# Optimization experiments

Measured on AMD Instinct MI355X. Metric: run time of the kernel, lower is better.

Reference implementation:

```python
import jax, jax.numpy as jnp
import numpy as np

EPS = 1e-6  # torch.nn.CosineSimilarity eps


def setup_inputs() -> dict:
    key = jax.random.key(0)
    k1, k2, k3, k4 = jax.random.split(key, 4)
    B, S, I, H, P = 16, 512, 512, 512, 16
    hidden = jax.random.normal(k1, (B, S, I), dtype=jnp.float32)
    # per-prototype linear weights (no bias); torch Linear stores (out, in)
    W1 = jax.random.normal(k2, (P, H, I), dtype=jnp.float32) / np.sqrt(I)
    W2 = jax.random.normal(k3, (P, H, H), dtype=jnp.float32) / np.sqrt(H)
    protos = jax.random.normal(k4, (P, H), dtype=jnp.float32)  # torch.randn(1,H) per proto
    return {"hidden": hidden, "W1": W1, "W2": W2, "protos": protos}


def reference(hidden, W1, W2, protos):
    # Batched version of the per-prototype loop:
    # layer1: ReLU(hidden @ W1[p].T) -> [B,S,P,H]
    h1 = jax.nn.relu(jnp.einsum("bsi,phi->bsph", hidden, W1))
    # layer2: ReLU(h1 @ W2[p].T) -> [B,S,P,H]
    h2 = jax.nn.relu(jnp.einsum("bsph,pgh->bspg", h1, W2))
    # cosine similarity along feature dim vs. each prototype vector
    dot = jnp.einsum("bsph,ph->bsp", h2, protos)
    xn = jnp.maximum(jnp.linalg.norm(h2, axis=-1), EPS)          # [B,S,P]
    pn = jnp.maximum(jnp.linalg.norm(protos, axis=-1), EPS)      # [P]
    cos_scores = dot / (xn * pn)                                  # [B,S,P]
    return cos_scores
```

## Files before the change

### kernel.cpp

```cpp
#include <hip/hip_runtime.h>
#include <hip/hip_bf16.h>

#define R_TOT 8192
#define DIM   512
#define NP    16
#define EPSV  1e-6f

typedef __bf16 bf16x8 __attribute__((ext_vector_type(8)));
typedef float  f32x16 __attribute__((ext_vector_type(16)));

__device__ __forceinline__ unsigned int f2bf(float f) {
  unsigned int u = __float_as_uint(f);
  return (u + 0x7FFFu + ((u >> 16) & 1u)) >> 16;
}
__device__ __forceinline__ unsigned int pack2(float a, float b) {
  return f2bf(a) | (f2bf(b) << 16);
}
__device__ __forceinline__ f32x16 zero16() {
  f32x16 z;
  #pragma unroll
  for (int i = 0; i < 16; ++i) z[i] = 0.f;
  return z;
}

__global__ void cvt_x_kernel(const float* __restrict__ X, unsigned short* __restrict__ Xb) {
  int t   = blockIdx.x * 256 + threadIdx.x;
  int row = t >> 6;
  int c   = t & 63;
  const float4* src = (const float4*)(X + (size_t)row * DIM + c * 8);
  float4 f0 = src[0], f1 = src[1];
  uint4 o;
  o.x = pack2(f0.x, f0.y);
  o.y = pack2(f0.z, f0.w);
  o.z = pack2(f1.x, f1.y);
  o.w = pack2(f1.z, f1.w);
  *(uint4*)(Xb + (size_t)row * DIM + 8 * (c ^ (row & 7))) = o;
}

__global__ void pack_w_kernel(const float* __restrict__ W, unsigned short* __restrict__ Wp) {
  int t  = blockIdx.x * 256 + threadIdx.x;
  int l  = t & 63;
  int kk = (t >> 6) & 31;
  int mt = (t >> 11) & 15;
  int p  = t >> 15;
  int row = mt * 32 + (l & 31);
  int k0  = 16 * kk + 8 * (l >> 5);
  const float4* s = (const float4*)(W + ((size_t)p * DIM + row) * DIM + k0);
  float4 f0 = s[0], f1 = s[1];
  uint4 o;
  o.x = pack2(f0.x, f0.y);
  o.y = pack2(f0.z, f0.w);
  o.z = pack2(f1.x, f1.y);
  o.w = pack2(f1.z, f1.w);
  *(uint4*)(Wp + (size_t)t * 8) = o;
}

__global__ void proto_norm_kernel(const float* __restrict__ protos, float* __restrict__ pn) {
  int p = blockIdx.x;
  int l = threadIdx.x;
  float ss = 0.f;
  #pragma unroll
  for (int k = 0; k < DIM / 64; ++k) {
    float v = protos[p * DIM + k * 64 + l];
    ss += v * v;
  }
  #pragma unroll
  for (int m = 32; m >= 1; m >>= 1) ss += __shfl_xor(ss, m, 64);
  if (l == 0) pn[p] = fmaxf(sqrtf(ss), EPSV);
}

__device__ __forceinline__ void gemm_stage32(const unsigned short* tile,
                                             const unsigned short* __restrict__ Wpk,
                                             f32x16 acc[2][2],
                                             int l, int l31, int h) {
  for (int kk = 0; kk < 32; ++kk) {
    bf16x8 a[2], b[2];
    #pragma unroll
    for (int mi = 0; mi < 2; ++mi)
      a[mi] = *(const bf16x8*)(Wpk + (size_t)mi * 16384 + kk * 512 + l * 8);
    #pragma unroll
    for (int nt = 0; nt < 2; ++nt) {
      int token = nt * 32 + l31;
      int boff  = (32 * kk + 16 * h) ^ ((token & 7) << 4);
      b[nt] = *(const bf16x8*)((const char*)tile + token * 1024 + boff);
    }
    #pragma unroll
    for (int mi = 0; mi < 2; ++mi)
      #pragma unroll
      for (int nt = 0; nt < 2; ++nt)
        acc[mi][nt] = __builtin_amdgcn_mfma_f32_32x32x16_bf16(a[mi], b[nt], acc[mi][nt], 0, 0, 0);
  }
}

__global__ __launch_bounds__(512, 4) void fused_kernel(
    const unsigned short* __restrict__ Xb,
    const unsigned short* __restrict__ W1p,
    const unsigned short* __restrict__ W2p,
    const float* __restrict__ protos,
    const float* __restrict__ pn,
    float* __restrict__ out) {
  __shared__ unsigned short tile[64 * DIM];
  __shared__ float red[8][64][2];

  const int raw = blockIdx.x;
  const int bid = (raw & 7) * 256 + (raw >> 3);
  const int p   = bid >> 7;
  const int r0  = (bid & 127) << 6;
  const int tid = threadIdx.x;
  const int w   = tid >> 6;
  const int l   = tid & 63;
  const int l31 = l & 31;
  const int h   = l >> 5;

  {
    const uint4* g = (const uint4*)(Xb + (size_t)r0 * DIM);
    uint4* s = (uint4*)tile;
    #pragma unroll
    for (int it = 0; it < 8; ++it) s[tid + it * 512] = g[tid + it * 512];
  }
  __syncthreads();

  f32x16 acc[2][2];
  #pragma unroll
  for (int mi = 0; mi < 2; ++mi)
    #pragma unroll
    for (int nt = 0; nt < 2; ++nt) acc[mi][nt] = zero16();

  gemm_stage32(tile, W1p + ((size_t)p * 16 + 2 * w) * 16384, acc, l, l31, h);

  __syncthreads();

  #pragma unroll
  for (int mi = 0; mi < 2; ++mi)
    #pragma unroll
    for (int nt = 0; nt < 2; ++nt) {
      int token = nt * 32 + l31;
      #pragma unroll
      for (int g = 0; g < 4; ++g) {
        uint2 pk;
        pk.x = pack2(fmaxf(acc[mi][nt][4 * g + 0], 0.f), fmaxf(acc[mi][nt][4 * g + 1], 0.f));
        pk.y = pack2(fmaxf(acc[mi][nt][4 * g + 2], 0.f), fmaxf(acc[mi][nt][4 * g + 3], 0.f));
        int featb = 128 * w + 64 * mi + 16 * g + 8 * h;
        *(uint2*)((char*)tile + token * 1024 + (featb ^ ((token & 7) << 4))) = pk;
      }
    }
  __syncthreads();

  #pragma unroll
  for (int mi = 0; mi < 2; ++mi)
    #pragma unroll
    for (int nt = 0; nt < 2; ++nt) acc[mi][nt] = zero16();

  gemm_stage32(tile, W2p + ((size_t)p * 16 + 2 * w) * 16384, acc, l, l31, h);

  #pragma unroll
  for (int nt = 0; nt < 2; ++nt) {
    float d = 0.f, ssq = 0.f;
    #pragma unroll
    for (int mi = 0; mi < 2; ++mi)
      #pragma unroll
      for (int g = 0; g < 4; ++g) {
        float4 pv = *(const float4*)(protos + p * DIM + 64 * w + 32 * mi + 8 * g + 4 * h);
        #pragma unroll
        for (int j = 0; j < 4; ++j) {
          float hv = fmaxf(acc[mi][nt][4 * g + j], 0.f);
          d   += hv * ((const float*)&pv)[j];
          ssq += hv * hv;
        }
      }
    d   += __shfl_xor(d, 32, 64);
    ssq += __shfl_xor(ssq, 32, 64);
    if (l < 32) {
      red[w][nt * 32 + l31][0] = d;
      red[w][nt * 32 + l31][1] = ssq;
    }
  }
  __syncthreads();

  if (tid < 64) {
    float d = 0.f, ssq = 0.f;
    #pragma unroll
    for (int ww = 0; ww < 8; ++ww) {
      d   += red[ww][tid][0];
      ssq += red[ww][tid][1];
    }
    float xn = fmaxf(sqrtf(ssq), EPSV);
    out[(size_t)(r0 + tid) * NP + p] = d / (xn * pn[p]);
  }
}

extern "C" void kernel_launch(void* const* d_in, const int* in_sizes, int n_in,
                              void* d_out, int out_size, void* d_ws, size_t ws_size,
                              hipStream_t stream) {
  const float* X      = (const float*)d_in[0];
  const float* W1     = (const float*)d_in[1];
  const float* W2     = (const float*)d_in[2];
  const float* protos = (const float*)d_in[3];
  float* out = (float*)d_out;

  unsigned short* Xb  = (unsigned short*)d_ws;
  unsigned short* W1p = Xb  + (size_t)R_TOT * DIM;
  unsigned short* W2p = W1p + (size_t)NP * DIM * DIM;
  float* pn = (float*)(W2p + (size_t)NP * DIM * DIM);

  cvt_x_kernel<<<2048, 256, 0, stream>>>(X, Xb);
  pack_w_kernel<<<2048, 256, 0, stream>>>(W1, W1p);
  pack_w_kernel<<<2048, 256, 0, stream>>>(W2, W2p);
  proto_norm_kernel<<<NP, 64, 0, stream>>>(protos, pn);
  fused_kernel<<<2048, 512, 0, stream>>>(Xb, W1p, W2p, protos, pn, out);
}
```

Before: 165.8 us.

## Double token tile to 128 rows and software-pipeline GEMM operand loads

Each block now processes 128 token rows instead of 64, so every weight fragment loaded from global memory feeds four MFMA tiles rather than two. This halves the weight traffic per output and the grid shrinks to 1024 blocks. The k-loop also prefetches A and B fragments two steps ahead through a 3-deep register ring. The reduction scratch now reuses the tile buffer after a barrier. In exchange the shared tile grows to 128 KB, occupancy bound drops to 2 blocks, and register pressure rises with 8 accumulators plus prefetch buffers.

```diff
diff --git a/kernel.cpp b/kernel.cpp
--- a/kernel.cpp
+++ b/kernel.cpp
@@ -71,41 +71,58 @@
 
 __device__ __forceinline__ void gemm_stage32(const unsigned short* tile,
                                              const unsigned short* __restrict__ Wpk,
-                                             f32x16 acc[2][2],
+                                             f32x16 acc[2][4],
                                              int l, int l31, int h) {
+  const char* tbase = (const char*)tile;
+  bf16x8 a[3][2], b[3][4];
+  #pragma unroll
+  for (int pp = 0; pp < 2; ++pp) {
+    #pragma unroll
+    for (int mi = 0; mi < 2; ++mi)
+      a[pp][mi] = *(const bf16x8*)(Wpk + (size_t)mi * 16384 + pp * 512 + l * 8);
+    #pragma unroll
+    for (int nt = 0; nt < 4; ++nt) {
+      int token = nt * 32 + l31;
+      int boff  = (32 * pp + 16 * h) ^ ((token & 7) << 4);
+      b[pp][nt] = *(const bf16x8*)(tbase + token * 1024 + boff);
+    }
+  }
+  #pragma unroll
   for (int kk = 0; kk < 32; ++kk) {
-    bf16x8 a[2], b[2];
+    const int cur = kk % 3;
+    const int nxt = (kk + 2) % 3;
+    if (kk + 2 < 32) {
+      #pragma unroll
+      for (int mi = 0; mi < 2; ++mi)
+        a[nxt][mi] = *(const bf16x8*)(Wpk + (size_t)mi * 16384 + (kk + 2) * 512 + l * 8);
+      #pragma unroll
+      for (int nt = 0; nt < 4; ++nt) {
+        int token = nt * 32 + l31;
+        int boff  = (32 * (kk + 2) + 16 * h) ^ ((token & 7) << 4);
+        b[nxt][nt] = *(const bf16x8*)(tbase + token * 1024 + boff);
+      }
+    }
     #pragma unroll
     for (int mi = 0; mi < 2; ++mi)
-      a[mi] = *(const bf16x8*)(Wpk + (size_t)mi * 16384 + kk * 512 + l * 8);
-    #pragma unroll
-    for (int nt = 0; nt < 2; ++nt) {
-      int token = nt * 32 + l31;
-      int boff  = (32 * kk + 16 * h) ^ ((token & 7) << 4);
-      b[nt] = *(const bf16x8*)((const char*)tile + token * 1024 + boff);
-    }
-    #pragma unroll
-    for (int mi = 0; mi < 2; ++mi)
-      #pragma unroll
-      for (int nt = 0; nt < 2; ++nt)
-        acc[mi][nt] = __builtin_amdgcn_mfma_f32_32x32x16_bf16(a[mi], b[nt], acc[mi][nt], 0, 0, 0);
-  }
-}
-
-__global__ __launch_bounds__(512, 4) void fused_kernel(
+      #pragma unroll
+      for (int nt = 0; nt < 4; ++nt)
+        acc[mi][nt] = __builtin_amdgcn_mfma_f32_32x32x16_bf16(a[cur][mi], b[cur][nt], acc[mi][nt], 0, 0, 0);
+  }
+}
+
+__global__ __launch_bounds__(512, 2) void fused_kernel(
     const unsigned short* __restrict__ Xb,
     const unsigned short* __restrict__ W1p,
     const unsigned short* __restrict__ W2p,
     const float* __restrict__ protos,
     const float* __restrict__ pn,
     float* __restrict__ out) {
-  __shared__ unsigned short tile[64 * DIM];
-  __shared__ float red[8][64][2];
+  __shared__ unsigned short tile[128 * DIM];
 
   const int raw = blockIdx.x;
-  const int bid = (raw & 7) * 256 + (raw >> 3);
-  const int p   = bid >> 7;
-  const int r0  = (bid & 127) << 6;
+  const int bid = (raw & 7) * 128 + (raw >> 3);
+  const int p   = bid >> 6;
+  const int r0  = (bid & 63) << 7;
   const int tid = threadIdx.x;
   const int w   = tid >> 6;
   const int l   = tid & 63;
@@ -114,17 +131,17 @@
 
   {
     const uint4* g = (const uint4*)(Xb + (size_t)r0 * DIM);
-    uint4* s = (uint4*)tile;
-    #pragma unroll
-    for (int it = 0; it < 8; ++it) s[tid + it * 512] = g[tid + it * 512];
-  }
-  __syncthreads();
-
-  f32x16 acc[2][2];
+    uint4* sm = (uint4*)tile;
+    #pragma unroll
+    for (int it = 0; it < 16; ++it) sm[tid + it * 512] = g[tid + it * 512];
+  }
+  __syncthreads();
+
+  f32x16 acc[2][4];
   #pragma unroll
   for (int mi = 0; mi < 2; ++mi)
     #pragma unroll
-    for (int nt = 0; nt < 2; ++nt) acc[mi][nt] = zero16();
+    for (int nt = 0; nt < 4; ++nt) acc[mi][nt] = zero16();
 
   gemm_stage32(tile, W1p + ((size_t)p * 16 + 2 * w) * 16384, acc, l, l31, h);
 
@@ -133,14 +150,14 @@
   #pragma unroll
   for (int mi = 0; mi < 2; ++mi)
     #pragma unroll
-    for (int nt = 0; nt < 2; ++nt) {
+    for (int nt = 0; nt < 4; ++nt) {
       int token = nt * 32 + l31;
       #pragma unroll
-      for (int g = 0; g < 4; ++g) {
+      for (int gg = 0; gg < 4; ++gg) {
         uint2 pk;
-        pk.x = pack2(fmaxf(acc[mi][nt][4 * g + 0], 0.f), fmaxf(acc[mi][nt][4 * g + 1], 0.f));
-        pk.y = pack2(fmaxf(acc[mi][nt][4 * g + 2], 0.f), fmaxf(acc[mi][nt][4 * g + 3], 0.f));
-        int featb = 128 * w + 64 * mi + 16 * g + 8 * h;
+        pk.x = pack2(fmaxf(acc[mi][nt][4 * gg + 0], 0.f), fmaxf(acc[mi][nt][4 * gg + 1], 0.f));
+        pk.y = pack2(fmaxf(acc[mi][nt][4 * gg + 2], 0.f), fmaxf(acc[mi][nt][4 * gg + 3], 0.f));
+        int featb = 128 * w + 64 * mi + 16 * gg + 8 * h;
         *(uint2*)((char*)tile + token * 1024 + (featb ^ ((token & 7) << 4))) = pk;
       }
     }
@@ -149,40 +166,48 @@
   #pragma unroll
   for (int mi = 0; mi < 2; ++mi)
     #pragma unroll
-    for (int nt = 0; nt < 2; ++nt) acc[mi][nt] = zero16();
+    for (int nt = 0; nt < 4; ++nt) acc[mi][nt] = zero16();
 
   gemm_stage32(tile, W2p + ((size_t)p * 16 + 2 * w) * 16384, acc, l, l31, h);
 
-  #pragma unroll
-  for (int nt = 0; nt < 2; ++nt) {
+  float dv[4], sv[4];
+  #pragma unroll
+  for (int nt = 0; nt < 4; ++nt) {
     float d = 0.f, ssq = 0.f;
     #pragma unroll
     for (int mi = 0; mi < 2; ++mi)
       #pragma unroll
-      for (int g = 0; g < 4; ++g) {
-        float4 pv = *(const float4*)(protos + p * DIM + 64 * w + 32 * mi + 8 * g + 4 * h);
+      for (int gg = 0; gg < 4; ++gg) {
+        float4 pv = *(const float4*)(protos + p * DIM + 64 * w + 32 * mi + 8 * gg + 4 * h);
         #pragma unroll
         for (int j = 0; j < 4; ++j) {
-          float hv = fmaxf(acc[mi][nt][4 * g + j], 0.f);
+          float hv = fmaxf(acc[mi][nt][4 * gg + j], 0.f);
           d   += hv * ((const float*)&pv)[j];
           ssq += hv * hv;
         }
       }
     d   += __shfl_xor(d, 32, 64);
     ssq += __shfl_xor(ssq, 32, 64);
+    dv[nt] = d;
+    sv[nt] = ssq;
+  }
+
+  __syncthreads();
+  float* red = (float*)tile;
+  #pragma unroll
+  for (int nt = 0; nt < 4; ++nt)
     if (l < 32) {
-      red[w][nt * 32 + l31][0] = d;
-      red[w][nt * 32 + l31][1] = ssq;
-    }
-  }
-  __syncthreads();
-
-  if (tid < 64) {
+      red[(w * 128 + nt * 32 + l31) * 2 + 0] = dv[nt];
+      red[(w * 128 + nt * 32 + l31) * 2 + 1] = sv[nt];
+    }
+  __syncthreads();
+
+  if (tid < 128) {
     float d = 0.f, ssq = 0.f;
     #pragma unroll
     for (int ww = 0; ww < 8; ++ww) {
-      d   += red[ww][tid][0];
-      ssq += red[ww][tid][1];
+      d   += red[(ww * 128 + tid) * 2 + 0];
+      ssq += red[(ww * 128 + tid) * 2 + 1];
     }
     float xn = fmaxf(sqrtf(ssq), EPSV);
     out[(size_t)(r0 + tid) * NP + p] = d / (xn * pn[p]);
@@ -207,5 +232,5 @@
   pack_w_kernel<<<2048, 256, 0, stream>>>(W1, W1p);
   pack_w_kernel<<<2048, 256, 0, stream>>>(W2, W2p);
   proto_norm_kernel<<<NP, 64, 0, stream>>>(protos, pn);
-  fused_kernel<<<2048, 512, 0, stream>>>(Xb, W1p, W2p, protos, pn, out);
-}
+  fused_kernel<<<1024, 512, 0, stream>>>(Xb, W1p, W2p, protos, pn, out);
+}
```

New measurement: 215.9 us. 30.2% more time.
